# Kernel optimization log

Measured on AMD Instinct MI355X. Metric: run time of the kernel, lower is better.

Reference implementation:

```python
import jax, jax.numpy as jnp
import numpy as np

WD = 11
HF = WD // 2  # 5

def _offsets():
    # Reproduce the torch module's expanding-ring offset ordering exactly.
    offs = []
    for i in range(1, HF + 1):
        for v in range(HF - i, HF + i + 1):
            for u in range(HF - i, HF + i + 1):
                if not (u == HF and v == HF) and (u, v) not in offs:
                    offs.append((u, v))
    return offs  # length WD*WD-1 = 120

_OFFS = _offsets()


def setup_inputs() -> dict:
    key = jax.random.key(0)
    x = jax.random.normal(key, (2, 3, 384, 1280), dtype=jnp.float32)
    return {"x": x, "attack": 1}


def reference(x, attack):
    n, c, h, w = x.shape
    xm = jnp.mean(x, axis=1)  # [n,h,w] grayscale
    xp = jnp.pad(xm, ((0, 0), (HF, HF), (HF, HF)), mode="reflect")  # [n,h+2*HF,w+2*HF]
    # All 120 shifted views in ring order; static slices, stacked on channel dim.
    shifted = jnp.stack([xp[:, v:v + h, u:u + w] for (u, v) in _OFFS], axis=1)  # [n,120,h,w]
    center = xm[:, None, :, :]
    if attack:
        return jax.nn.sigmoid((shifted - center) * 100000.0)
    return shifted >= center
```

## Files before the change

kernel.cpp:

```cpp
#include <hip/hip_runtime.h>
#include <cstddef>
#include <cstdint>

constexpr int N_  = 2;
constexpr int C_  = 3;
constexpr int H_  = 384;
constexpr int W_  = 1280;
constexpr int HWp = H_ * W_;
constexpr int NOFF = 120;
constexpr int HF_  = 5;

constexpr int TW = 256;
constexpr int TH = 4;
constexpr int SW = TW + 2 * HF_;
constexpr int SH = TH + 2 * HF_;

__host__ __device__ constexpr int k_of(int u, int v) {
    int du = u - HF_, dv = v - HF_;
    int au = du < 0 ? -du : du;
    int av = dv < 0 ? -dv : dv;
    int r = au > av ? au : av;
    if (r == 0) return -1;
    int base = (2 * r - 1) * (2 * r - 1) - 1;
    int dv2 = v - (HF_ - r);
    int du2 = u - (HF_ - r);
    int idx = 0;
    if (dv2 == 0)            idx = du2;
    else if (dv2 == 2 * r)   idx = (2 * r + 1) + 2 * (2 * r - 1) + du2;
    else                     idx = (2 * r + 1) + 2 * (dv2 - 1) + (du2 == 0 ? 0 : 1);
    return base + idx;
}

__device__ __forceinline__ float census_val(float s, float center) {
    float d = s - center;
    float r;
    if (__builtin_expect(fabsf(d) >= 1.6e-4f, 1)) {
        r = d > 0.0f ? 1.0f : 0.0f;
    } else {
        float e = __expf(d * -100000.0f);
        r = __builtin_amdgcn_rcpf(1.0f + e);
    }
    return r;
}

typedef float f32x4 __attribute__((ext_vector_type(4)));

__global__ __launch_bounds__(256) void census_fused_lds(const float* __restrict__ x,
                                                        float* __restrict__ out) {
    __shared__ float sm[SH][SW];

    int bx = blockIdx.x % (W_ / TW);
    int t  = blockIdx.x / (W_ / TW);
    int yt = t % (H_ / TH);
    int n  = t / (H_ / TH);
    int x0 = bx * TW, y0 = yt * TH;

    const float* xn = x + (size_t)n * C_ * HWp;

    for (int idx = threadIdx.x; idx < SH * SW; idx += 256) {
        int r = idx / SW, c = idx - r * SW;
        int gy = y0 + r - HF_;
        gy = gy < 0 ? -gy : gy;
        gy = gy >= H_ ? 2 * (H_ - 1) - gy : gy;
        int gx = x0 + c - HF_;
        gx = gx < 0 ? -gx : gx;
        gx = gx >= W_ ? 2 * (W_ - 1) - gx : gx;
        int off = gy * W_ + gx;
        sm[r][c] = (xn[off] + xn[off + HWp] + xn[off + 2 * HWp]) / 3.0f;
    }
    __syncthreads();

    int ty = threadIdx.x >> 6;
    int tx = (threadIdx.x & 63) * 4;
    int y  = y0 + ty;
    int xg = x0 + tx;

    float4 c4;
    c4.x = sm[HF_ + ty][HF_ + tx + 0];
    c4.y = sm[HF_ + ty][HF_ + tx + 1];
    c4.z = sm[HF_ + ty][HF_ + tx + 2];
    c4.w = sm[HF_ + ty][HF_ + tx + 3];

    float* outp = out + (size_t)n * NOFF * HWp + (size_t)y * W_ + xg;

#pragma unroll
    for (int v = 0; v < 11; ++v) {
        const float* srow = sm[ty + v];

        float s[14];
#pragma unroll
        for (int j = 0; j < 14; ++j) s[j] = srow[tx + j];

#pragma unroll
        for (int u = 0; u < 11; ++u) {
            if (u == HF_ && v == HF_) continue;
            const int k = k_of(u, v);
            f32x4 r;
            r.x = census_val(s[u + 0], c4.x);
            r.y = census_val(s[u + 1], c4.y);
            r.z = census_val(s[u + 2], c4.z);
            r.w = census_val(s[u + 3], c4.w);
            __builtin_nontemporal_store(r, (f32x4*)(outp + (size_t)k * HWp));
        }
    }
}

extern "C" void kernel_launch(void* const* d_in, const int* in_sizes, int n_in,
                              void* d_out, int out_size, void* d_ws, size_t ws_size,
                              hipStream_t stream) {
    const float* x = (const float*)d_in[0];
    float* out = (float*)d_out;

    const int blocks = N_ * (H_ / TH) * (W_ / TW);
    census_fused_lds<<<blocks, 256, 0, stream>>>(x, out);
}
```

Baseline: 476.8 us.

## Split into mean prepass and per-offset-plane census kernel with contiguous writes

Adds a separate kernel that computes the channel mean into workspace, then a census kernel where each block handles one offset plane and a contiguous span of pixels. Each block writes one output plane contiguously instead of scattering 120 strided stores per thread. This is meant to improve write locality and DRAM efficiency for the large output. In exchange it adds an extra launch and workspace round trip, and the mean is re-read 120 times through gathered, unaligned scalar loads. The old fused kernel is kept as a fallback when workspace is too small.

```diff
diff --git a/kernel.cpp b/kernel.cpp
--- a/kernel.cpp
+++ b/kernel.cpp
@@ -9,11 +9,6 @@
 constexpr int HWp = H_ * W_;
 constexpr int NOFF = 120;
 constexpr int HF_  = 5;
-
-constexpr int TW = 256;
-constexpr int TH = 4;
-constexpr int SW = TW + 2 * HF_;
-constexpr int SH = TH + 2 * HF_;
 
 __host__ __device__ constexpr int k_of(int u, int v) {
     int du = u - HF_, dv = v - HF_;
@@ -31,6 +26,37 @@
     return base + idx;
 }
 
+struct OffTab { int du[NOFF]; int dv[NOFF]; };
+constexpr OffTab make_offtab() {
+    OffTab t{};
+    for (int v = 0; v < 11; ++v)
+        for (int u = 0; u < 11; ++u) {
+            int k = k_of(u, v);
+            if (k >= 0) { t.du[k] = u - HF_; t.dv[k] = v - HF_; }
+        }
+    return t;
+}
+constexpr OffTab OT = make_offtab();
+
+__global__ __launch_bounds__(256) void mean_kernel(const float* __restrict__ x,
+                                                   float* __restrict__ xm) {
+    int i = blockIdx.x * 256 + threadIdx.x;
+    constexpr int TOT4 = N_ * HWp / 4;
+    if (i >= TOT4) return;
+    int n = i / (HWp / 4);
+    int j = i - n * (HWp / 4);
+    const float4* x0 = (const float4*)(x + (size_t)n * C_ * HWp);
+    const float4* x1 = (const float4*)(x + (size_t)n * C_ * HWp + HWp);
+    const float4* x2 = (const float4*)(x + (size_t)n * C_ * HWp + 2 * HWp);
+    float4 a = x0[j], b = x1[j], c = x2[j];
+    float4 m;
+    m.x = (a.x + b.x + c.x) / 3.0f;
+    m.y = (a.y + b.y + c.y) / 3.0f;
+    m.z = (a.z + b.z + c.z) / 3.0f;
+    m.w = (a.w + b.w + c.w) / 3.0f;
+    ((float4*)xm)[i] = m;
+}
+
 __device__ __forceinline__ float census_val(float s, float center) {
     float d = s - center;
     float r;
@@ -44,6 +70,72 @@
 }
 
 typedef float f32x4 __attribute__((ext_vector_type(4)));
+
+constexpr int SPB  = 8;
+constexpr int SPAN = HWp / SPB;
+constexpr int ITER = SPAN / (256 * 4);
+
+struct Px { float4 c; float s0, s1, s2, s3; };
+
+__device__ __forceinline__ Px load_px(const float* __restrict__ xmn,
+                                      int p, int du, int dv) {
+    Px q;
+    int y = p / W_;
+    int x = p - y * W_;
+    int sy = y + dv;
+    sy = sy < 0 ? -sy : sy;
+    sy = sy >= H_ ? 2 * (H_ - 1) - sy : sy;
+    const float* srow = xmn + (size_t)sy * W_;
+    q.c = *(const float4*)(xmn + (size_t)y * W_ + x);
+    int sx0 = x + du;
+#pragma unroll
+    for (int i = 0; i < 4; ++i) {
+        int sx = sx0 + i;
+        sx = sx < 0 ? -sx : sx;
+        sx = sx >= W_ ? 2 * (W_ - 1) - sx : sx;
+        (&q.s0)[i] = srow[sx];
+    }
+    return q;
+}
+
+__global__ __launch_bounds__(256) void census_plane(const float* __restrict__ xm,
+                                                    float* __restrict__ out) {
+    int b    = blockIdx.x;
+    int span = b & (SPB - 1);
+    int t    = b >> 3;
+    int k    = t % NOFF;
+    int n    = t / NOFF;
+    int du   = OT.du[k], dv = OT.dv[k];
+
+    const float* xmn  = xm + (size_t)n * HWp;
+    float*       outp = out + ((size_t)(n * NOFF + k)) * HWp;
+
+    int p = span * SPAN + (int)threadIdx.x * 4;
+    Px cur = load_px(xmn, p, du, dv);
+#pragma unroll 4
+    for (int it = 0; it < ITER - 1; ++it) {
+        Px nxt = load_px(xmn, p + 1024, du, dv);
+        f32x4 r;
+        r.x = census_val(cur.s0, cur.c.x);
+        r.y = census_val(cur.s1, cur.c.y);
+        r.z = census_val(cur.s2, cur.c.z);
+        r.w = census_val(cur.s3, cur.c.w);
+        __builtin_nontemporal_store(r, (f32x4*)(outp + p));
+        p += 1024;
+        cur = nxt;
+    }
+    f32x4 r;
+    r.x = census_val(cur.s0, cur.c.x);
+    r.y = census_val(cur.s1, cur.c.y);
+    r.z = census_val(cur.s2, cur.c.z);
+    r.w = census_val(cur.s3, cur.c.w);
+    __builtin_nontemporal_store(r, (f32x4*)(outp + p));
+}
+
+constexpr int TW = 256;
+constexpr int TH = 4;
+constexpr int SW = TW + 2 * HF_;
+constexpr int SH = TH + 2 * HF_;
 
 __global__ __launch_bounds__(256) void census_fused_lds(const float* __restrict__ x,
                                                         float* __restrict__ out) {
@@ -86,11 +178,9 @@
 #pragma unroll
     for (int v = 0; v < 11; ++v) {
         const float* srow = sm[ty + v];
-
         float s[14];
 #pragma unroll
         for (int j = 0; j < 14; ++j) s[j] = srow[tx + j];
-
 #pragma unroll
         for (int u = 0; u < 11; ++u) {
             if (u == HF_ && v == HF_) continue;
@@ -111,6 +201,16 @@
     const float* x = (const float*)d_in[0];
     float* out = (float*)d_out;
 
-    const int blocks = N_ * (H_ / TH) * (W_ / TW);
-    census_fused_lds<<<blocks, 256, 0, stream>>>(x, out);
-}
+    const size_t xm_bytes = (size_t)N_ * HWp * sizeof(float);
+
+    if (ws_size >= xm_bytes) {
+        float* xm = (float*)d_ws;
+        const int mean_blocks = (N_ * HWp / 4 + 255) / 256;
+        mean_kernel<<<mean_blocks, 256, 0, stream>>>(x, xm);
+        const int plane_blocks = N_ * NOFF * SPB;
+        census_plane<<<plane_blocks, 256, 0, stream>>>(xm, out);
+    } else {
+        const int census_blocks = N_ * (H_ / TH) * (W_ / TW);
+        census_fused_lds<<<census_blocks, 256, 0, stream>>>(x, out);
+    }
+}
```

New measurement: 516.9 us. +8.4%, slower.
